# Optimization experiments

Measured on AMD Instinct MI355X. Metric: run time of the kernel, lower is better.

## Reference

```python
import jax, jax.numpy as jnp
import numpy as np

B, N_OBS = 4096, 64
H = 256
SCALE = 0.05  # keep activations stable through SQUARE/MUL layers


def setup_inputs() -> dict:
    key = jax.random.key(0)
    ks = jax.random.split(key, 16)
    rn = lambda k, shp, s=SCALE: s * jax.random.normal(k, shp, dtype=jnp.float32)
    return {
        "x": jax.random.normal(ks[0], (B, N_OBS), dtype=jnp.float32),
        "xdot": jax.random.normal(ks[1], (B, N_OBS), dtype=jnp.float32),
        "w1": rn(ks[2], (H, N_OBS)), "b1": rn(ks[3], (H,)),
        "w2a": rn(ks[4], (H, H)), "b2a": rn(ks[5], (H,)),
        "w2b": rn(ks[6], (H, H)), "b2b": rn(ks[7], (H,)),
        "w3a": rn(ks[8], (H, H)), "b3a": rn(ks[9], (H,)),
        "w3s": rn(ks[10], (H, N_OBS)), "b3s": rn(ks[11], (H,)),
        "wout": rn(ks[12], (1, H)),
        "scalar": jax.random.normal(ks[13], (1,), dtype=jnp.float32),
    }


def reference(x, xdot, w1, b1, w2a, b2a, w2b, b2b, w3a, b3a, w3s, b3s, wout, scalar):
    # mul path: empty mul_activation -> yy = x*0 + scalar  (shape [B, n_obs])
    yy = x * 0 + scalar

    # Layer 1: SQUARE. Initial jac is identity, so
    # matmul(2*diag(z), W1) @ I == 2*z[:,:,None] * W1
    z = x @ w1.T + b1                      # [B, H]
    y = z * z
    jac = (2.0 * z)[:, :, None] * w1[None]  # [B, H, N_OBS]

    # Layer 2: MUL. diag(z1)@W2b + diag(z2)@W2a == z1[:,:,None]*w2b + z2[:,:,None]*w2a
    z1 = y @ w2a.T + b2a
    z2 = y @ w2b.T + b2b
    y = z1 * z2
    grad = z1[:, :, None] * w2b[None] + z2[:, :, None] * w2a[None]  # [B, H, H]
    jac = jnp.einsum('boh,bhi->boi', grad, jac)                      # [B, H, N_OBS]

    # Layer 3: SKIP. jac = diag(z1)@W3s + (diag(z2)@W3a)@jac
    z1 = y @ w3a.T + b3a
    z2 = x @ w3s.T + b3s
    y = z1 * z2
    jac = z1[:, :, None] * w3s[None] + z2[:, :, None] * jnp.einsum('oh,bhi->boi', w3a, jac)

    numerical_b = y @ wout.T                                # [B, 1]
    jac = jnp.einsum('oh,bhi->boi', wout, jac)              # [B, 1, N_OBS]
    numerical_bdot = jnp.sum(jac[:, 0, :] * xdot, axis=1)   # [B]
    return (numerical_b, numerical_bdot, y, yy)
```

## Files before the change

kernel.cpp:

```cpp
#include <hip/hip_runtime.h>

typedef unsigned short ushort_t;
typedef unsigned int uint_t;
typedef __bf16 bf16x8 __attribute__((ext_vector_type(8)));
typedef float f32x4 __attribute__((ext_vector_type(4)));

#define H 256
#define RPB 32
#define NBLK 128

#define NB_OFF 0
#define BDOT_OFF 4096
#define Y_OFF 8192
#define YY_OFF (8192 + 4096 * 256)

__device__ __forceinline__ ushort_t f2bf(float x) {
    union { float f; uint_t u; } c; c.f = x;
    uint_t r = (c.u + 0x7FFFu + ((c.u >> 16) & 1u)) >> 16;
    return (ushort_t)r;
}
__device__ __forceinline__ float bf2f(ushort_t v) {
    union { uint_t u; float f; } c; c.u = ((uint_t)v) << 16;
    return c.f;
}

#define O_W1b  0
#define O_W1T  16384
#define O_W2ab 32768
#define O_W2bb 98304
#define O_W3ab 163840
#define O_W2aT 229376
#define O_W2bT 294912
#define O_W3aT 360448
#define O_W3sb 425984
#define O_W3sT 442368

__global__ __launch_bounds__(256) void prep_weights(
    const float* __restrict__ w1, const float* __restrict__ w2a,
    const float* __restrict__ w2b, const float* __restrict__ w3a,
    const float* __restrict__ w3s, const float* __restrict__ wout,
    ushort_t* __restrict__ ws) {
    __shared__ float tile[32][65];
    int b = blockIdx.x;
    const float* src; int Oo, Ot, C, t; bool scl;
    if (b < 32)       { src = w2a; Oo = O_W2ab; Ot = O_W2aT; C = 256; t = b;       scl = false; }
    else if (b < 64)  { src = w2b; Oo = O_W2bb; Ot = O_W2bT; C = 256; t = b - 32;  scl = false; }
    else if (b < 96)  { src = w3a; Oo = O_W3ab; Ot = O_W3aT; C = 256; t = b - 64;  scl = true;  }
    else if (b < 104) { src = w1;  Oo = O_W1b;  Ot = O_W1T;  C = 64;  t = b - 96;  scl = false; }
    else              { src = w3s; Oo = O_W3sb; Ot = O_W3sT; C = 64;  t = b - 104; scl = true;  }
    int tr, tc;
    if (C == 256) { tr = t >> 2; tc = t & 3; } else { tr = t; tc = 0; }
    int r0 = tr * 32, c0 = tc * 64;
    const int tid = threadIdx.x;

    union pack8 { ushort_t u[8]; uint4 q; };
    {
        int r = tid >> 3, c8 = (tid & 7) << 3;
        const float* s = src + (r0 + r) * C + c0 + c8;
        pack8 p;
#pragma unroll
        for (int j = 0; j < 8; j++) { float v = s[j]; tile[r][c8 + j] = v; p.u[j] = f2bf(v); }
        *(uint4*)(ws + Oo + (r0 + r) * C + c0 + c8) = p.q;
    }
    __syncthreads();
    {
        int cc = tid >> 2, r8 = (tid & 3) << 3;
        pack8 p;
#pragma unroll
        for (int j = 0; j < 8; j++) {
            float v = tile[r8 + j][cc];
            if (scl) v *= wout[r0 + r8 + j];
            p.u[j] = f2bf(v);
        }
        *(uint4*)(ws + Ot + (c0 + cc) * 256 + r0 + r8) = p.q;
    }
}

#define RS 4
#define RA 4
#define U_RING 0
#define U_Y    32768
#define U_Z12  40960
#define U_Z22  49152
#define U_Z23  57344
#define U_U    65536
#define U_XD   73728
#define U_NB   77824
#define SMEM_USHORTS 77888
#define SMEM_BYTES (SMEM_USHORTS * 2)

__device__ __forceinline__ void gload16(const ushort_t* g, ushort_t* l) {
    __builtin_amdgcn_global_load_lds(
        (const __attribute__((address_space(1))) void*)g,
        (__attribute__((address_space(3))) void*)l, 16, 0, 0);
}

template <int N> __device__ __forceinline__ void vwait() {
    if constexpr (N == 3) asm volatile("s_waitcnt vmcnt(3)" ::: "memory");
    else if constexpr (N == 2) asm volatile("s_waitcnt vmcnt(2)" ::: "memory");
    else if constexpr (N == 1) asm volatile("s_waitcnt vmcnt(1)" ::: "memory");
    else asm volatile("s_waitcnt vmcnt(0)" ::: "memory");
}

#define PHASE_BARRIER() do { \
    asm volatile("s_waitcnt lgkmcnt(0)" ::: "memory"); \
    __builtin_amdgcn_sched_barrier(0); \
    __builtin_amdgcn_s_barrier(); \
    __builtin_amdgcn_sched_barrier(0); \
} while (0)

__device__ __forceinline__ int posw(int r, int c) { return r * H + (c ^ ((r & 7) << 3)); }

template <int P, bool SUM>
__device__ __forceinline__ void ring_phase(
    const ushort_t* __restrict__ gm0, const ushort_t* __restrict__ gm1,
    const ushort_t* __restrict__ gn0, const ushort_t* __restrict__ gn1,
    const ushort_t* aM0, const ushort_t* aM1,
    ushort_t* rw, int srcoff, int boff, int kq, int sw,
    f32x4& a00, f32x4& a01, f32x4& a10, f32x4& a11) {
    const int arow0 = ( boff >> 5) * H;
    const int arow1 = arow0 + 16 * H;
#pragma unroll
    for (int k = 0; k < 16; ++k) {
        const int u = P * 16 + k;
        if (P == 2) {
            if (k < 13) vwait<3>();
            else if (k == 13) vwait<2>();
            else if (k == 14) vwait<1>();
            else vwait<0>();
        } else {
            vwait<3>();
        }
        __builtin_amdgcn_sched_barrier(0);
        bf16x8 b = *(const bf16x8*)(rw + (u & 3) * 512 + boff);
        const ushort_t* am = (k & 1) ? aM1 : aM0;
        const int ko = (((k >> 1) << 5) + kq) ^ sw;
        bf16x8 a0 = *(const bf16x8*)(am + arow0 + ko);
        bf16x8 a1 = *(const bf16x8*)(am + arow1 + ko);
        if (u + RA < 48) {
            asm volatile("s_waitcnt lgkmcnt(2)" ::: "memory");
            __builtin_amdgcn_sched_barrier(0);
            const int k4 = k + RA;
            const ushort_t* g = (k4 < 16) ? ((k4 & 1) ? gm1 : gm0)
                                          : ((k4 & 1) ? gn1 : gn0);
            const int cc = (k4 & 15) >> 1;
            gload16(g + srcoff + (cc << 5), rw + ((u + RA) & 3) * 512);
        }
        if ((k & 1) == 0 || SUM) {
            a00 = __builtin_amdgcn_mfma_f32_16x16x32_bf16(a0, b, a00, 0, 0, 0);
            a01 = __builtin_amdgcn_mfma_f32_16x16x32_bf16(a1, b, a01, 0, 0, 0);
        } else {
            a10 = __builtin_amdgcn_mfma_f32_16x16x32_bf16(a0, b, a10, 0, 0, 0);
            a11 = __builtin_amdgcn_mfma_f32_16x16x32_bf16(a1, b, a11, 0, 0, 0);
        }
    }
}

template <int NF, int STRA, int STRB>
__device__ __forceinline__ void gemm_one(const ushort_t* sA, const ushort_t* __restrict__ B0,
                                         int lane, int k0, f32x4& acc0) {
    const int row = lane & 15;
    const int kq = (lane >> 4) << 3;
    const int sw = (row & 7) << 3;
    bf16x8 b0[NF], a[NF];
    const ushort_t* bp0 = B0 + row * STRB + k0 + kq;
    const ushort_t* ap = sA + row * STRA;
#pragma unroll
    for (int i = 0; i < NF; i++) b0[i] = *(const bf16x8*)(bp0 + i * 32);
#pragma unroll
    for (int i = 0; i < NF; i++) a[i] = *(const bf16x8*)(ap + ((k0 + i * 32 + kq) ^ sw));
    __builtin_amdgcn_sched_barrier(0);
#pragma unroll
    for (int i = 0; i < NF; i++)
        acc0 = __builtin_amdgcn_mfma_f32_16x16x32_bf16(a[i], b0[i], acc0, 0, 0, 0);
}

__global__ __launch_bounds__(1024) void net_main(
    const float* __restrict__ x, const float* __restrict__ xd,
    const float* __restrict__ b1, const float* __restrict__ b2a,
    const float* __restrict__ b2b, const float* __restrict__ b3a,
    const float* __restrict__ b3s, const float* __restrict__ wout,
    const float* __restrict__ scalar, const ushort_t* __restrict__ ws,
    float* __restrict__ out) {
    extern __shared__ __align__(16) ushort_t smem[];
    ushort_t* sY   = smem + U_Y;
    ushort_t* sZ12 = smem + U_Z12;
    ushort_t* sZ22 = smem + U_Z22;
    ushort_t* sZ23 = smem + U_Z23;
    ushort_t* sU   = smem + U_U;
    float* sXd = (float*)(smem + U_XD);
    float* sNB = (float*)(smem + U_NB);

    const int tid = threadIdx.x;
    const int wid = tid >> 6;
    const int lane = tid & 63;
    const int row16 = lane & 15;
    const int rq = lane >> 4;
    const int R0 = blockIdx.x * RPB;
    const int n0 = wid * 16;
    const int kq = rq << 3;
    const int sw = (row16 & 7) << 3;

    ushort_t* rw = smem + U_RING + wid * (RS * 512);
    const int nsrc = (wid << 4) + (lane >> 2);
    const int srcoff = nsrc * 256 + (((lane & 3) ^ (nsrc & 3)) << 3);
    const int boff = row16 * 32 + (kq ^ ((row16 & 3) << 3));

    const ushort_t* gW2ab = ws + O_W2ab;
    const ushort_t* gW2bb = ws + O_W2bb;
    const ushort_t* gW3ab = ws + O_W3ab;
    const ushort_t* gW3aT = ws + O_W3aT;
    const ushort_t* gW2bT = ws + O_W2bT;
    const ushort_t* gW2aT = ws + O_W2aT;

    f32x4 zk0, zk1, y3k0, y3k1;

    {
        float sc = scalar[0];
        int xr = tid >> 6, xc = tid & 63;
        float xd0 = xd[(R0 + xr) * 64 + xc];
        float xd1 = xd[(R0 + 16 + xr) * 64 + xc];
        out[YY_OFF + (R0 + xr) * 64 + xc] = sc;
        out[YY_OFF + (R0 + 16 + xr) * 64 + xc] = sc;
        const ushort_t* w1p = ws + O_W1b + (n0 + row16) * 64 + kq;
        const ushort_t* w3p = ws + O_W3sb + (n0 + row16) * 64 + kq;
        bf16x8 pb0 = *(const bf16x8*)(w1p);
        bf16x8 pb1 = *(const bf16x8*)(w1p + 32);
        bf16x8 pb2 = *(const bf16x8*)(w3p);
        bf16x8 pb3 = *(const bf16x8*)(w3p + 32);
        const float* xg0 = x + (R0 + row16) * 64;
        const float* xg1 = x + (R0 + 16 + row16) * 64;
        float4 xa0 = *(const float4*)(xg0 + kq);
        float4 xa1 = *(const float4*)(xg0 + kq + 4);
        float4 xa2 = *(const float4*)(xg0 + 32 + kq);
        float4 xa3 = *(const float4*)(xg0 + 32 + kq + 4);
        float4 xb0 = *(const float4*)(xg1 + kq);
        float4 xb1 = *(const float4*)(xg1 + kq + 4);
        float4 xb2 = *(const float4*)(xg1 + 32 + kq);
        float4 xb3 = *(const float4*)(xg1 + 32 + kq + 4);
        __builtin_amdgcn_sched_barrier(0);
        gload16(gW2ab + srcoff, rw);
        gload16(gW2bb + srcoff, rw + 512);
        gload16(gW2ab + srcoff + 32, rw + 1024);
        gload16(gW2bb + srcoff + 32, rw + 1536);
        __builtin_amdgcn_sched_barrier(0);
        sXd[tid] = xd0;
        sXd[tid + 1024] = xd1;
        if (tid < RPB) sNB[tid] = 0.f;
        union { ushort_t u[8]; bf16x8 v; } A0, A1, B0v, B1v;
#pragma unroll
        for (int j = 0; j < 4; j++) {
            A0.u[j]      = f2bf(((const float*)&xa0)[j]);
            A0.u[4 + j]  = f2bf(((const float*)&xa1)[j]);
            A1.u[j]      = f2bf(((const float*)&xa2)[j]);
            A1.u[4 + j]  = f2bf(((const float*)&xa3)[j]);
            B0v.u[j]     = f2bf(((const float*)&xb0)[j]);
            B0v.u[4 + j] = f2bf(((const float*)&xb1)[j]);
            B1v.u[j]     = f2bf(((const float*)&xb2)[j]);
            B1v.u[4 + j] = f2bf(((const float*)&xb3)[j]);
        }
        f32x4 z0 = {0.f,0.f,0.f,0.f}, z1 = {0.f,0.f,0.f,0.f};
        f32x4 q0 = {0.f,0.f,0.f,0.f}, q1 = {0.f,0.f,0.f,0.f};
        z0 = __builtin_amdgcn_mfma_f32_16x16x32_bf16(A0.v, pb0, z0, 0, 0, 0);
        z0 = __builtin_amdgcn_mfma_f32_16x16x32_bf16(A1.v, pb1, z0, 0, 0, 0);
        z1 = __builtin_amdgcn_mfma_f32_16x16x32_bf16(B0v.v, pb0, z1, 0, 0, 0);
        z1 = __builtin_amdgcn_mfma_f32_16x16x32_bf16(B1v.v, pb1, z1, 0, 0, 0);
        q0 = __builtin_amdgcn_mfma_f32_16x16x32_bf16(A0.v, pb2, q0, 0, 0, 0);
        q0 = __builtin_amdgcn_mfma_f32_16x16x32_bf16(A1.v, pb3, q0, 0, 0, 0);
        q1 = __builtin_amdgcn_mfma_f32_16x16x32_bf16(B0v.v, pb2, q1, 0, 0, 0);
        q1 = __builtin_amdgcn_mfma_f32_16x16x32_bf16(B1v.v, pb3, q1, 0, 0, 0);
        int c = n0 + row16;
        float bz = b1[c], bs = b3s[c];
#pragma unroll
        for (int i = 0; i < 4; i++) {
            int r = rq * 4 + i;
            int p0 = posw(r, c), p1 = posw(r + 16, c);
            float za = z0[i] + bz, zb = z1[i] + bz;
            zk0[i] = za; zk1[i] = zb;
            sY[p0] = f2bf(za * za);
            sY[p1] = f2bf(zb * zb);
            sZ23[p0] = f2bf(q0[i] + bs);
            sZ23[p1] = f2bf(q1[i] + bs);
        }
    }
    PHASE_BARRIER();

    {
        f32x4 a00 = {0.f,0.f,0.f,0.f}, a01 = {0.f,0.f,0.f,0.f};
        f32x4 a10 = {0.f,0.f,0.f,0.f}, a11 = {0.f,0.f,0.f,0.f};
        ring_phase<0, false>(gW2ab, gW2bb, gW3ab, gW3aT, sY, sY,
                             rw, srcoff, boff, kq, sw, a00, a01, a10, a11);
        int c = n0 + row16;
        float ba = b2a[c], bb = b2b[c];
#pragma unroll
        for (int i = 0; i < 4; i++) {
            int r = rq * 4 + i;
            int p0 = posw(r, c), p1 = posw(r + 16, c);
            float z12a = a00[i] + ba, z22a = a10[i] + bb;
            float z12b = a01[i] + ba, z22b = a11[i] + bb;
            sZ12[p0] = f2bf(z12a); sZ22[p0] = f2bf(z22a); sU[p0] = f2bf(z12a * z22a);
            sZ12[p1] = f2bf(z12b); sZ22[p1] = f2bf(z22b); sU[p1] = f2bf(z12b * z22b);
        }
    }
    PHASE_BARRIER();

    {
        f32x4 zz0 = {0.f,0.f,0.f,0.f}, zz1 = {0.f,0.f,0.f,0.f};
        f32x4 tt0 = {0.f,0.f,0.f,0.f}, tt1 = {0.f,0.f,0.f,0.f};
        ring_phase<1, false>(gW3ab, gW3aT, gW2bT, gW2aT, sU, sZ23,
                             rw, srcoff, boff, kq, sw, zz0, zz1, tt0, tt1);
        int c = n0 + row16;
        float ba = b3a[c], wo = wout[c];
#pragma unroll
        for (int i = 0; i < 4; i++) {
            int r = rq * 4 + i;
            int p0 = posw(r, c), p1 = posw(r + 16, c);
            float z13a = zz0[i] + ba, z23a = bf2f(sZ23[p0]);
            float z13b = zz1[i] + ba, z23b = bf2f(sZ23[p1]);
            float y3a = z13a * z23a, y3b = z13b * z23b;
            y3k0[i] = y3a; y3k1[i] = y3b;
            sY[p0] = f2bf(z13a);
            sY[p1] = f2bf(z13b);
            sZ12[p0] = f2bf(tt0[i] * bf2f(sZ12[p0]));
            sZ22[p0] = f2bf(tt0[i] * bf2f(sZ22[p0]));
            sZ12[p1] = f2bf(tt1[i] * bf2f(sZ12[p1]));
            sZ22[p1] = f2bf(tt1[i] * bf2f(sZ22[p1]));
            float v0 = wo * y3a, v1 = wo * y3b;
            v0 += __shfl_xor(v0, 1); v0 += __shfl_xor(v0, 2);
            v0 += __shfl_xor(v0, 4); v0 += __shfl_xor(v0, 8);
            v1 += __shfl_xor(v1, 1); v1 += __shfl_xor(v1, 2);
            v1 += __shfl_xor(v1, 4); v1 += __shfl_xor(v1, 8);
            if (row16 == 0) { atomicAdd(&sNB[r], v0); atomicAdd(&sNB[r + 16], v1); }
        }
    }
    PHASE_BARRIER();

    {
        f32x4 pp0 = {0.f,0.f,0.f,0.f}, pp1 = {0.f,0.f,0.f,0.f};
        f32x4 d0 = {0.f,0.f,0.f,0.f}, d1 = {0.f,0.f,0.f,0.f};
        ring_phase<2, true>(gW2bT, gW2aT, gW2bT, gW2aT, sZ12, sZ22,
                            rw, srcoff, boff, kq, sw, pp0, pp1, d0, d1);
        int c = n0 + row16;
#pragma unroll
        for (int i = 0; i < 4; i++) {
            int r = rq * 4 + i;
            sU[posw(r, c)] = f2bf(2.f * pp0[i] * zk0[i]);
            sU[posw(r + 16, c)] = f2bf(2.f * pp1[i] * zk1[i]);
        }
    }
    PHASE_BARRIER();

    {
        int c = n0 + row16;
#pragma unroll
        for (int i = 0; i < 4; i++) {
            out[Y_OFF + (R0 + rq * 4 + i) * H + c] = y3k0[i];
            out[Y_OFF + (R0 + 16 + rq * 4 + i) * H + c] = y3k1[i];
        }
        int mat = wid >> 3, kh = (wid >> 2) & 1, nt = wid & 3;
        const ushort_t* Abase = mat ? sU : sY;
        const ushort_t* B = ws + (mat ? O_W1T : O_W3sT) + nt * 16 * H;
        float* dst = (float*)(mat ? sZ22 : sZ12) + kh * 2048;
        int cc = nt * 16 + row16;
#pragma unroll
        for (int rg = 0; rg < 2; rg++) {
            f32x4 acc = {0.f,0.f,0.f,0.f};
            gemm_one<4, H, H>(Abase + rg * 16 * H, B, lane, kh * 128, acc);
#pragma unroll
            for (int i = 0; i < 4; i++)
                dst[(rg * 16 + rq * 4 + i) * 64 + cc] = acc[i];
        }
    }
    PHASE_BARRIER();

    {
        float* F0 = (float*)sZ12;
        float* F1 = F0 + 2048;
        float* F2 = (float*)sZ22;
        float* F3 = F2 + 2048;
        int r = tid >> 5, j = tid & 31;
        int e = r * 64 + j, e2 = e + 32;
        float s = (F0[e] + F1[e] + F2[e] + F3[e]) * sXd[e] +
                  (F0[e2] + F1[e2] + F2[e2] + F3[e2]) * sXd[e2];
        s += __shfl_xor(s, 1);
        s += __shfl_xor(s, 2);
        s += __shfl_xor(s, 4);
        s += __shfl_xor(s, 8);
        s += __shfl_xor(s, 16);
        if (j == 0) out[BDOT_OFF + R0 + r] = s;
        if (tid < RPB) out[NB_OFF + R0 + tid] = sNB[tid];
    }
}

extern "C" void kernel_launch(void* const* d_in, const int* in_sizes, int n_in,
                              void* d_out, int out_size, void* d_ws, size_t ws_size,
                              hipStream_t stream) {
    (void)in_sizes; (void)n_in; (void)out_size; (void)ws_size;
    const float* x = (const float*)d_in[0];
    const float* xd = (const float*)d_in[1];
    const float* w1 = (const float*)d_in[2];
    const float* b1 = (const float*)d_in[3];
    const float* w2a = (const float*)d_in[4];
    const float* b2a = (const float*)d_in[5];
    const float* w2b = (const float*)d_in[6];
    const float* b2b = (const float*)d_in[7];
    const float* w3a = (const float*)d_in[8];
    const float* b3a = (const float*)d_in[9];
    const float* w3s = (const float*)d_in[10];
    const float* b3s = (const float*)d_in[11];
    const float* wout = (const float*)d_in[12];
    const float* scalar = (const float*)d_in[13];
    ushort_t* ws = (ushort_t*)d_ws;
    float* out = (float*)d_out;

    static bool attr_set = false;
    if (!attr_set) {
        hipFuncSetAttribute((const void*)net_main,
                            hipFuncAttributeMaxDynamicSharedMemorySize, SMEM_BYTES);
        attr_set = true;
    }

    prep_weights<<<112, 256, 0, stream>>>(w1, w2a, w2b, w3a, w3s, wout, ws);
    net_main<<<NBLK, 1024, SMEM_BYTES, stream>>>(x, xd, b1, b2a, b2b, b3a, b3s, wout, scalar, ws, out);
}
```

Baseline: 35.33 us.

## Split each row tile across paired blocks exchanging partials via global flags

The grid doubles from 128 to 256 blocks. Each 32-row tile is now handled by a pair of blocks, one for the even (z1) matrices and one for the odd (z2) matrices. The two blocks exchange intermediates (y1, z22, t, z13, partial products, partial Jacobian) through a global workspace and synchronise with acquire/release flags that prep_weights clears. The aim is to halve per-block GEMM work and use more compute units, at the cost of global-memory round trips, spin-waiting, and a deadlock risk if the paired blocks are not co-resident.

```diff
diff --git a/kernel.cpp b/kernel.cpp
--- a/kernel.cpp
+++ b/kernel.cpp
@@ -7,7 +7,8 @@
 
 #define H 256
 #define RPB 32
-#define NBLK 128
+#define PAIRS 128
+#define NBLK 256
 
 #define NB_OFF 0
 #define BDOT_OFF 4096
@@ -34,14 +35,36 @@
 #define O_W3aT 360448
 #define O_W3sb 425984
 #define O_W3sT 442368
+#define X_EX   458752
+#define PXU    61440
+#define EX_Y1  0
+#define EX_Z23 8192
+#define EX_Z22 16384
+#define EX_T   24576
+#define EX_Z13 32768
+#define EX_PO  40960
+#define EX_FJ  57344
+#define X_FLAG (X_EX + PAIRS * PXU)
+#define FE1 0
+#define FE2 1
+#define FO2 2
+#define FO3 3
+#define FO4 4
+#define FO5 5
 
 __global__ __launch_bounds__(256) void prep_weights(
     const float* __restrict__ w1, const float* __restrict__ w2a,
     const float* __restrict__ w2b, const float* __restrict__ w3a,
     const float* __restrict__ w3s, const float* __restrict__ wout,
     ushort_t* __restrict__ ws) {
+    int b = blockIdx.x;
+    const int tid = threadIdx.x;
+    if (b == 112) {
+        int* fl = (int*)(ws + X_FLAG);
+        for (int i = tid; i < PAIRS * 8; i += 256) fl[i] = 0;
+        return;
+    }
     __shared__ float tile[32][65];
-    int b = blockIdx.x;
     const float* src; int Oo, Ot, C, t; bool scl;
     if (b < 32)       { src = w2a; Oo = O_W2ab; Ot = O_W2aT; C = 256; t = b;       scl = false; }
     else if (b < 64)  { src = w2b; Oo = O_W2bb; Ot = O_W2bT; C = 256; t = b - 32;  scl = false; }
@@ -51,7 +74,6 @@
     int tr, tc;
     if (C == 256) { tr = t >> 2; tc = t & 3; } else { tr = t; tc = 0; }
     int r0 = tr * 32, c0 = tc * 64;
-    const int tid = threadIdx.x;
 
     union pack8 { ushort_t u[8]; uint4 q; };
     {
@@ -76,17 +98,13 @@
     }
 }
 
-#define RS 4
-#define RA 4
 #define U_RING 0
-#define U_Y    32768
-#define U_Z12  40960
-#define U_Z22  49152
-#define U_Z23  57344
-#define U_U    65536
-#define U_XD   73728
-#define U_NB   77824
-#define SMEM_USHORTS 77888
+#define U_B0   32768
+#define U_B1   40960
+#define U_B2   49152
+#define U_XD   57344
+#define U_NB   61440
+#define SMEM_USHORTS 61504
 #define SMEM_BYTES (SMEM_USHORTS * 2)
 
 __device__ __forceinline__ void gload16(const ushort_t* g, ushort_t* l) {
@@ -109,50 +127,54 @@
     __builtin_amdgcn_sched_barrier(0); \
 } while (0)
 
+__device__ __forceinline__ void post_flag(int* f) {
+    __syncthreads();
+    if (threadIdx.x == 0)
+        __hip_atomic_store(f, 1, __ATOMIC_RELEASE, __HIP_MEMORY_SCOPE_AGENT);
+}
+__device__ __forceinline__ void wait_flag(int* f) {
+    if (threadIdx.x == 0) {
+        while (__hip_atomic_load(f, __ATOMIC_ACQUIRE, __HIP_MEMORY_SCOPE_AGENT) == 0)
+            __builtin_amdgcn_s_sleep(2);
+    }
+    __syncthreads();
+}
+
 __device__ __forceinline__ int posw(int r, int c) { return r * H + (c ^ ((r & 7) << 3)); }
 
-template <int P, bool SUM>
-__device__ __forceinline__ void ring_phase(
-    const ushort_t* __restrict__ gm0, const ushort_t* __restrict__ gm1,
-    const ushort_t* __restrict__ gn0, const ushort_t* __restrict__ gn1,
-    const ushort_t* aM0, const ushort_t* aM1,
-    ushort_t* rw, int srcoff, int boff, int kq, int sw,
-    f32x4& a00, f32x4& a01, f32x4& a10, f32x4& a11) {
-    const int arow0 = ( boff >> 5) * H;
+template <int PH>
+__device__ __forceinline__ void ring8(
+    const ushort_t* __restrict__ mA, const ushort_t* __restrict__ mB,
+    const ushort_t* __restrict__ mC,
+    const ushort_t* aM, ushort_t* rw, int srcoff, int boff, int row16,
+    int kq, int sw, f32x4& acc0, f32x4& acc1) {
+    const int arow0 = row16 * H;
     const int arow1 = arow0 + 16 * H;
 #pragma unroll
-    for (int k = 0; k < 16; ++k) {
-        const int u = P * 16 + k;
-        if (P == 2) {
-            if (k < 13) vwait<3>();
-            else if (k == 13) vwait<2>();
-            else if (k == 14) vwait<1>();
+    for (int k = 0; k < 8; ++k) {
+        const int u = PH * 8 + k;
+        if (PH == 2) {
+            if (k < 5) vwait<3>();
+            else if (k == 5) vwait<2>();
+            else if (k == 6) vwait<1>();
             else vwait<0>();
         } else {
             vwait<3>();
         }
         __builtin_amdgcn_sched_barrier(0);
         bf16x8 b = *(const bf16x8*)(rw + (u & 3) * 512 + boff);
-        const ushort_t* am = (k & 1) ? aM1 : aM0;
-        const int ko = (((k >> 1) << 5) + kq) ^ sw;
-        bf16x8 a0 = *(const bf16x8*)(am + arow0 + ko);
-        bf16x8 a1 = *(const bf16x8*)(am + arow1 + ko);
-        if (u + RA < 48) {
+        const int ko = ((k << 5) + kq) ^ sw;
+        bf16x8 a0 = *(const bf16x8*)(aM + arow0 + ko);
+        bf16x8 a1 = *(const bf16x8*)(aM + arow1 + ko);
+        if (u + 4 < 24) {
             asm volatile("s_waitcnt lgkmcnt(2)" ::: "memory");
             __builtin_amdgcn_sched_barrier(0);
-            const int k4 = k + RA;
-            const ushort_t* g = (k4 < 16) ? ((k4 & 1) ? gm1 : gm0)
-                                          : ((k4 & 1) ? gn1 : gn0);
-            const int cc = (k4 & 15) >> 1;
-            gload16(g + srcoff + (cc << 5), rw + ((u + RA) & 3) * 512);
-        }
-        if ((k & 1) == 0 || SUM) {
-            a00 = __builtin_amdgcn_mfma_f32_16x16x32_bf16(a0, b, a00, 0, 0, 0);
-            a01 = __builtin_amdgcn_mfma_f32_16x16x32_bf16(a1, b, a01, 0, 0, 0);
-        } else {
-            a10 = __builtin_amdgcn_mfma_f32_16x16x32_bf16(a0, b, a10, 0, 0, 0);
-            a11 = __builtin_amdgcn_mfma_f32_16x16x32_bf16(a1, b, a11, 0, 0, 0);
-        }
+            const int u4 = u + 4;
+            const ushort_t* g = (u4 < 8) ? mA : (u4 < 16) ? mB : mC;
+            gload16(g + srcoff + ((u4 & 7) << 5), rw + (u4 & 3) * 512);
+        }
+        acc0 = __builtin_amdgcn_mfma_f32_16x16x32_bf16(a0, b, acc0, 0, 0, 0);
+        acc1 = __builtin_amdgcn_mfma_f32_16x16x32_bf16(a1, b, acc1, 0, 0, 0);
     }
 }
 
@@ -180,215 +202,338 @@
     const float* __restrict__ b1, const float* __restrict__ b2a,
     const float* __restrict__ b2b, const float* __restrict__ b3a,
     const float* __restrict__ b3s, const float* __restrict__ wout,
-    const float* __restrict__ scalar, const ushort_t* __restrict__ ws,
+    const float* __restrict__ scalar, ushort_t* __restrict__ ws,
     float* __restrict__ out) {
     extern __shared__ __align__(16) ushort_t smem[];
-    ushort_t* sY   = smem + U_Y;
-    ushort_t* sZ12 = smem + U_Z12;
-    ushort_t* sZ22 = smem + U_Z22;
-    ushort_t* sZ23 = smem + U_Z23;
-    ushort_t* sU   = smem + U_U;
+    ushort_t* sB0 = smem + U_B0;
+    ushort_t* sB1 = smem + U_B1;
+    ushort_t* sB2 = smem + U_B2;
     float* sXd = (float*)(smem + U_XD);
     float* sNB = (float*)(smem + U_NB);
+    float* sFJ = (float*)smem;
 
     const int tid = threadIdx.x;
     const int wid = tid >> 6;
     const int lane = tid & 63;
     const int row16 = lane & 15;
     const int rq = lane >> 4;
-    const int R0 = blockIdx.x * RPB;
+    const bool isE = blockIdx.x < PAIRS;
+    const int pid = blockIdx.x & (PAIRS - 1);
+    const int R0 = pid * RPB;
     const int n0 = wid * 16;
     const int kq = rq << 3;
     const int sw = (row16 & 7) << 3;
 
-    ushort_t* rw = smem + U_RING + wid * (RS * 512);
+    ushort_t* rw = smem + U_RING + wid * 2048;
     const int nsrc = (wid << 4) + (lane >> 2);
     const int srcoff = nsrc * 256 + (((lane & 3) ^ (nsrc & 3)) << 3);
     const int boff = row16 * 32 + (kq ^ ((row16 & 3) << 3));
 
-    const ushort_t* gW2ab = ws + O_W2ab;
-    const ushort_t* gW2bb = ws + O_W2bb;
-    const ushort_t* gW3ab = ws + O_W3ab;
-    const ushort_t* gW3aT = ws + O_W3aT;
-    const ushort_t* gW2bT = ws + O_W2bT;
-    const ushort_t* gW2aT = ws + O_W2aT;
-
-    f32x4 zk0, zk1, y3k0, y3k1;
-
-    {
-        float sc = scalar[0];
-        int xr = tid >> 6, xc = tid & 63;
-        float xd0 = xd[(R0 + xr) * 64 + xc];
-        float xd1 = xd[(R0 + 16 + xr) * 64 + xc];
-        out[YY_OFF + (R0 + xr) * 64 + xc] = sc;
-        out[YY_OFF + (R0 + 16 + xr) * 64 + xc] = sc;
-        const ushort_t* w1p = ws + O_W1b + (n0 + row16) * 64 + kq;
-        const ushort_t* w3p = ws + O_W3sb + (n0 + row16) * 64 + kq;
-        bf16x8 pb0 = *(const bf16x8*)(w1p);
-        bf16x8 pb1 = *(const bf16x8*)(w1p + 32);
-        bf16x8 pb2 = *(const bf16x8*)(w3p);
-        bf16x8 pb3 = *(const bf16x8*)(w3p + 32);
-        const float* xg0 = x + (R0 + row16) * 64;
-        const float* xg1 = x + (R0 + 16 + row16) * 64;
-        float4 xa0 = *(const float4*)(xg0 + kq);
-        float4 xa1 = *(const float4*)(xg0 + kq + 4);
-        float4 xa2 = *(const float4*)(xg0 + 32 + kq);
-        float4 xa3 = *(const float4*)(xg0 + 32 + kq + 4);
-        float4 xb0 = *(const float4*)(xg1 + kq);
-        float4 xb1 = *(const float4*)(xg1 + kq + 4);
-        float4 xb2 = *(const float4*)(xg1 + 32 + kq);
-        float4 xb3 = *(const float4*)(xg1 + 32 + kq + 4);
-        __builtin_amdgcn_sched_barrier(0);
-        gload16(gW2ab + srcoff, rw);
-        gload16(gW2bb + srcoff, rw + 512);
-        gload16(gW2ab + srcoff + 32, rw + 1024);
-        gload16(gW2bb + srcoff + 32, rw + 1536);
-        __builtin_amdgcn_sched_barrier(0);
-        sXd[tid] = xd0;
-        sXd[tid + 1024] = xd1;
-        if (tid < RPB) sNB[tid] = 0.f;
-        union { ushort_t u[8]; bf16x8 v; } A0, A1, B0v, B1v;
-#pragma unroll
-        for (int j = 0; j < 4; j++) {
-            A0.u[j]      = f2bf(((const float*)&xa0)[j]);
-            A0.u[4 + j]  = f2bf(((const float*)&xa1)[j]);
-            A1.u[j]      = f2bf(((const float*)&xa2)[j]);
-            A1.u[4 + j]  = f2bf(((const float*)&xa3)[j]);
-            B0v.u[j]     = f2bf(((const float*)&xb0)[j]);
-            B0v.u[4 + j] = f2bf(((const float*)&xb1)[j]);
-            B1v.u[j]     = f2bf(((const float*)&xb2)[j]);
-            B1v.u[4 + j] = f2bf(((const float*)&xb3)[j]);
-        }
-        f32x4 z0 = {0.f,0.f,0.f,0.f}, z1 = {0.f,0.f,0.f,0.f};
-        f32x4 q0 = {0.f,0.f,0.f,0.f}, q1 = {0.f,0.f,0.f,0.f};
-        z0 = __builtin_amdgcn_mfma_f32_16x16x32_bf16(A0.v, pb0, z0, 0, 0, 0);
-        z0 = __builtin_amdgcn_mfma_f32_16x16x32_bf16(A1.v, pb1, z0, 0, 0, 0);
-        z1 = __builtin_amdgcn_mfma_f32_16x16x32_bf16(B0v.v, pb0, z1, 0, 0, 0);
-        z1 = __builtin_amdgcn_mfma_f32_16x16x32_bf16(B1v.v, pb1, z1, 0, 0, 0);
-        q0 = __builtin_amdgcn_mfma_f32_16x16x32_bf16(A0.v, pb2, q0, 0, 0, 0);
-        q0 = __builtin_amdgcn_mfma_f32_16x16x32_bf16(A1.v, pb3, q0, 0, 0, 0);
-        q1 = __builtin_amdgcn_mfma_f32_16x16x32_bf16(B0v.v, pb2, q1, 0, 0, 0);
-        q1 = __builtin_amdgcn_mfma_f32_16x16x32_bf16(B1v.v, pb3, q1, 0, 0, 0);
-        int c = n0 + row16;
-        float bz = b1[c], bs = b3s[c];
-#pragma unroll
-        for (int i = 0; i < 4; i++) {
-            int r = rq * 4 + i;
-            int p0 = posw(r, c), p1 = posw(r + 16, c);
-            float za = z0[i] + bz, zb = z1[i] + bz;
-            zk0[i] = za; zk1[i] = zb;
-            sY[p0] = f2bf(za * za);
-            sY[p1] = f2bf(zb * zb);
-            sZ23[p0] = f2bf(q0[i] + bs);
-            sZ23[p1] = f2bf(q1[i] + bs);
-        }
-    }
-    PHASE_BARRIER();
-
-    {
-        f32x4 a00 = {0.f,0.f,0.f,0.f}, a01 = {0.f,0.f,0.f,0.f};
-        f32x4 a10 = {0.f,0.f,0.f,0.f}, a11 = {0.f,0.f,0.f,0.f};
-        ring_phase<0, false>(gW2ab, gW2bb, gW3ab, gW3aT, sY, sY,
-                             rw, srcoff, boff, kq, sw, a00, a01, a10, a11);
-        int c = n0 + row16;
-        float ba = b2a[c], bb = b2b[c];
-#pragma unroll
-        for (int i = 0; i < 4; i++) {
-            int r = rq * 4 + i;
-            int p0 = posw(r, c), p1 = posw(r + 16, c);
-            float z12a = a00[i] + ba, z22a = a10[i] + bb;
-            float z12b = a01[i] + ba, z22b = a11[i] + bb;
-            sZ12[p0] = f2bf(z12a); sZ22[p0] = f2bf(z22a); sU[p0] = f2bf(z12a * z22a);
-            sZ12[p1] = f2bf(z12b); sZ22[p1] = f2bf(z22b); sU[p1] = f2bf(z12b * z22b);
-        }
-    }
-    PHASE_BARRIER();
-
-    {
-        f32x4 zz0 = {0.f,0.f,0.f,0.f}, zz1 = {0.f,0.f,0.f,0.f};
-        f32x4 tt0 = {0.f,0.f,0.f,0.f}, tt1 = {0.f,0.f,0.f,0.f};
-        ring_phase<1, false>(gW3ab, gW3aT, gW2bT, gW2aT, sU, sZ23,
-                             rw, srcoff, boff, kq, sw, zz0, zz1, tt0, tt1);
-        int c = n0 + row16;
-        float ba = b3a[c], wo = wout[c];
-#pragma unroll
-        for (int i = 0; i < 4; i++) {
-            int r = rq * 4 + i;
-            int p0 = posw(r, c), p1 = posw(r + 16, c);
-            float z13a = zz0[i] + ba, z23a = bf2f(sZ23[p0]);
-            float z13b = zz1[i] + ba, z23b = bf2f(sZ23[p1]);
-            float y3a = z13a * z23a, y3b = z13b * z23b;
-            y3k0[i] = y3a; y3k1[i] = y3b;
-            sY[p0] = f2bf(z13a);
-            sY[p1] = f2bf(z13b);
-            sZ12[p0] = f2bf(tt0[i] * bf2f(sZ12[p0]));
-            sZ22[p0] = f2bf(tt0[i] * bf2f(sZ22[p0]));
-            sZ12[p1] = f2bf(tt1[i] * bf2f(sZ12[p1]));
-            sZ22[p1] = f2bf(tt1[i] * bf2f(sZ22[p1]));
-            float v0 = wo * y3a, v1 = wo * y3b;
-            v0 += __shfl_xor(v0, 1); v0 += __shfl_xor(v0, 2);
-            v0 += __shfl_xor(v0, 4); v0 += __shfl_xor(v0, 8);
-            v1 += __shfl_xor(v1, 1); v1 += __shfl_xor(v1, 2);
-            v1 += __shfl_xor(v1, 4); v1 += __shfl_xor(v1, 8);
-            if (row16 == 0) { atomicAdd(&sNB[r], v0); atomicAdd(&sNB[r + 16], v1); }
-        }
-    }
-    PHASE_BARRIER();
-
-    {
-        f32x4 pp0 = {0.f,0.f,0.f,0.f}, pp1 = {0.f,0.f,0.f,0.f};
-        f32x4 d0 = {0.f,0.f,0.f,0.f}, d1 = {0.f,0.f,0.f,0.f};
-        ring_phase<2, true>(gW2bT, gW2aT, gW2bT, gW2aT, sZ12, sZ22,
-                            rw, srcoff, boff, kq, sw, pp0, pp1, d0, d1);
-        int c = n0 + row16;
-#pragma unroll
-        for (int i = 0; i < 4; i++) {
-            int r = rq * 4 + i;
-            sU[posw(r, c)] = f2bf(2.f * pp0[i] * zk0[i]);
-            sU[posw(r + 16, c)] = f2bf(2.f * pp1[i] * zk1[i]);
-        }
-    }
-    PHASE_BARRIER();
-
-    {
-        int c = n0 + row16;
-#pragma unroll
-        for (int i = 0; i < 4; i++) {
-            out[Y_OFF + (R0 + rq * 4 + i) * H + c] = y3k0[i];
-            out[Y_OFF + (R0 + 16 + rq * 4 + i) * H + c] = y3k1[i];
-        }
-        int mat = wid >> 3, kh = (wid >> 2) & 1, nt = wid & 3;
-        const ushort_t* Abase = mat ? sU : sY;
-        const ushort_t* B = ws + (mat ? O_W1T : O_W3sT) + nt * 16 * H;
-        float* dst = (float*)(mat ? sZ22 : sZ12) + kh * 2048;
-        int cc = nt * 16 + row16;
-#pragma unroll
-        for (int rg = 0; rg < 2; rg++) {
-            f32x4 acc = {0.f,0.f,0.f,0.f};
-            gemm_one<4, H, H>(Abase + rg * 16 * H, B, lane, kh * 128, acc);
-#pragma unroll
-            for (int i = 0; i < 4; i++)
-                dst[(rg * 16 + rq * 4 + i) * 64 + cc] = acc[i];
-        }
-    }
-    PHASE_BARRIER();
-
-    {
-        float* F0 = (float*)sZ12;
-        float* F1 = F0 + 2048;
-        float* F2 = (float*)sZ22;
-        float* F3 = F2 + 2048;
-        int r = tid >> 5, j = tid & 31;
-        int e = r * 64 + j, e2 = e + 32;
-        float s = (F0[e] + F1[e] + F2[e] + F3[e]) * sXd[e] +
-                  (F0[e2] + F1[e2] + F2[e2] + F3[e2]) * sXd[e2];
-        s += __shfl_xor(s, 1);
-        s += __shfl_xor(s, 2);
-        s += __shfl_xor(s, 4);
-        s += __shfl_xor(s, 8);
-        s += __shfl_xor(s, 16);
-        if (j == 0) out[BDOT_OFF + R0 + r] = s;
-        if (tid < RPB) out[NB_OFF + R0 + tid] = sNB[tid];
+    ushort_t* ex = ws + X_EX + pid * PXU;
+    int* fl = (int*)(ws + X_FLAG) + pid * 8;
+
+    const int c = n0 + row16;
+
+    if (isE) {
+        const ushort_t* m0 = ws + O_W2ab;
+        const ushort_t* m1 = ws + O_W3ab;
+        const ushort_t* m2 = ws + O_W2bT;
+        f32x4 zk0, zk1;
+        {
+            const ushort_t* w1p = ws + O_W1b + c * 64 + kq;
+            bf16x8 pb0 = *(const bf16x8*)(w1p);
+            bf16x8 pb1 = *(const bf16x8*)(w1p + 32);
+            const float* xg0 = x + (R0 + row16) * 64;
+            const float* xg1 = x + (R0 + 16 + row16) * 64;
+            float4 xa0 = *(const float4*)(xg0 + kq);
+            float4 xa1 = *(const float4*)(xg0 + kq + 4);
+            float4 xa2 = *(const float4*)(xg0 + 32 + kq);
+            float4 xa3 = *(const float4*)(xg0 + 32 + kq + 4);
+            float4 xb0 = *(const float4*)(xg1 + kq);
+            float4 xb1 = *(const float4*)(xg1 + kq + 4);
+            float4 xb2 = *(const float4*)(xg1 + 32 + kq);
+            float4 xb3 = *(const float4*)(xg1 + 32 + kq + 4);
+            gload16(m0 + srcoff, rw);
+            gload16(m0 + srcoff + 32, rw + 512);
+            gload16(m0 + srcoff + 64, rw + 1024);
+            gload16(m0 + srcoff + 96, rw + 1536);
+            float sc = scalar[0];
+            {
+                int xr = tid >> 6, xc = tid & 63;
+                sXd[tid] = xd[(R0 + xr) * 64 + xc];
+                sXd[tid + 1024] = xd[(R0 + 16 + xr) * 64 + xc];
+                out[YY_OFF + (R0 + xr) * 64 + xc] = sc;
+                out[YY_OFF + (R0 + 16 + xr) * 64 + xc] = sc;
+                if (tid < RPB) sNB[tid] = 0.f;
+            }
+            union { ushort_t u[8]; bf16x8 v; } A0, A1, B0, B1;
+#pragma unroll
+            for (int j = 0; j < 4; j++) {
+                A0.u[j] = f2bf(((const float*)&xa0)[j]);
+                A0.u[4 + j] = f2bf(((const float*)&xa1)[j]);
+                A1.u[j] = f2bf(((const float*)&xa2)[j]);
+                A1.u[4 + j] = f2bf(((const float*)&xa3)[j]);
+                B0.u[j] = f2bf(((const float*)&xb0)[j]);
+                B0.u[4 + j] = f2bf(((const float*)&xb1)[j]);
+                B1.u[j] = f2bf(((const float*)&xb2)[j]);
+                B1.u[4 + j] = f2bf(((const float*)&xb3)[j]);
+            }
+            f32x4 z0 = {0.f,0.f,0.f,0.f}, z1 = {0.f,0.f,0.f,0.f};
+            z0 = __builtin_amdgcn_mfma_f32_16x16x32_bf16(A0.v, pb0, z0, 0, 0, 0);
+            z0 = __builtin_amdgcn_mfma_f32_16x16x32_bf16(A1.v, pb1, z0, 0, 0, 0);
+            z1 = __builtin_amdgcn_mfma_f32_16x16x32_bf16(B0.v, pb0, z1, 0, 0, 0);
+            z1 = __builtin_amdgcn_mfma_f32_16x16x32_bf16(B1.v, pb1, z1, 0, 0, 0);
+            float bz = b1[c];
+#pragma unroll
+            for (int i = 0; i < 4; i++) {
+                int r = rq * 4 + i;
+                float za = z0[i] + bz, zb = z1[i] + bz;
+                zk0[i] = za; zk1[i] = zb;
+                ushort_t ya = f2bf(za * za), yb = f2bf(zb * zb);
+                sB0[posw(r, c)] = ya; sB0[posw(r + 16, c)] = yb;
+                ex[EX_Y1 + r * H + c] = ya;
+                ex[EX_Y1 + (r + 16) * H + c] = yb;
+            }
+        }
+        post_flag(fl + FE1);
+
+        {
+            f32x4 a0 = {0.f,0.f,0.f,0.f}, a1 = {0.f,0.f,0.f,0.f};
+            ring8<0>(m0, m1, m2, sB0, rw, srcoff, boff, row16, kq, sw, a0, a1);
+            float ba = b2a[c];
+#pragma unroll
+            for (int i = 0; i < 4; i++) {
+                int r = rq * 4 + i;
+                sB1[posw(r, c)] = f2bf(a0[i] + ba);
+                sB1[posw(r + 16, c)] = f2bf(a1[i] + ba);
+            }
+        }
+        PHASE_BARRIER();
+        wait_flag(fl + FO2);
+        for (int e = tid; e < RPB * H; e += 1024) {
+            int r = e >> 8, cc2 = e & 255;
+            float z22 = bf2f(ex[EX_Z22 + e]);
+            int p = posw(r, cc2);
+            sB0[p] = f2bf(bf2f(sB1[p]) * z22);
+        }
+        PHASE_BARRIER();
+
+        f32x4 y3k0, y3k1;
+        {
+            f32x4 z0 = {0.f,0.f,0.f,0.f}, z1 = {0.f,0.f,0.f,0.f};
+            ring8<1>(m0, m1, m2, sB0, rw, srcoff, boff, row16, kq, sw, z0, z1);
+            float ba = b3a[c], wo = wout[c];
+#pragma unroll
+            for (int i = 0; i < 4; i++) {
+                int r = rq * 4 + i;
+                float z13a = z0[i] + ba, z13b = z1[i] + ba;
+                float z23a = bf2f(ex[EX_Z23 + r * H + c]);
+                float z23b = bf2f(ex[EX_Z23 + (r + 16) * H + c]);
+                float y3a = z13a * z23a, y3b = z13b * z23b;
+                y3k0[i] = y3a; y3k1[i] = y3b;
+                out[Y_OFF + (R0 + r) * H + c] = y3a;
+                out[Y_OFF + (R0 + 16 + r) * H + c] = y3b;
+                ex[EX_Z13 + r * H + c] = f2bf(z13a);
+                ex[EX_Z13 + (r + 16) * H + c] = f2bf(z13b);
+                float v0 = wo * y3a, v1 = wo * y3b;
+                v0 += __shfl_xor(v0, 1); v0 += __shfl_xor(v0, 2);
+                v0 += __shfl_xor(v0, 4); v0 += __shfl_xor(v0, 8);
+                v1 += __shfl_xor(v1, 1); v1 += __shfl_xor(v1, 2);
+                v1 += __shfl_xor(v1, 4); v1 += __shfl_xor(v1, 8);
+                if (row16 == 0) { atomicAdd(&sNB[r], v0); atomicAdd(&sNB[r + 16], v1); }
+            }
+        }
+        post_flag(fl + FE2);
+        wait_flag(fl + FO3);
+        {
+#pragma unroll
+            for (int i = 0; i < 4; i++) {
+                int r = rq * 4 + i;
+                int p0 = posw(r, c), p1 = posw(r + 16, c);
+                float t0 = bf2f(ex[EX_T + r * H + c]);
+                float t1 = bf2f(ex[EX_T + (r + 16) * H + c]);
+                sB1[p0] = f2bf(t0 * bf2f(sB1[p0]));
+                sB1[p1] = f2bf(t1 * bf2f(sB1[p1]));
+            }
+        }
+        PHASE_BARRIER();
+
+        {
+            f32x4 p0 = {0.f,0.f,0.f,0.f}, p1 = {0.f,0.f,0.f,0.f};
+            ring8<2>(m0, m1, m2, sB1, rw, srcoff, boff, row16, kq, sw, p0, p1);
+            wait_flag(fl + FO4);
+            const float* poF = (const float*)(ex + EX_PO);
+#pragma unroll
+            for (int i = 0; i < 4; i++) {
+                int r = rq * 4 + i;
+                float pa = p0[i] + poF[r * H + c];
+                float pb = p1[i] + poF[(r + 16) * H + c];
+                sB1[posw(r, c)] = f2bf(2.f * pa * zk0[i]);
+                sB1[posw(r + 16, c)] = f2bf(2.f * pb * zk1[i]);
+            }
+        }
+        PHASE_BARRIER();
+
+        {
+            int nt = wid & 3, kh = wid >> 2;
+            const ushort_t* B = ws + O_W1T + nt * 16 * H;
+            int cc2 = nt * 16 + row16;
+#pragma unroll
+            for (int rg = 0; rg < 2; rg++) {
+                f32x4 acc = {0.f,0.f,0.f,0.f};
+                gemm_one<2, H, H>(sB1 + rg * 16 * H, B, lane, kh * 64, acc);
+#pragma unroll
+                for (int i = 0; i < 4; i++)
+                    sFJ[kh * 2048 + (rg * 16 + rq * 4 + i) * 64 + cc2] = acc[i];
+            }
+        }
+        PHASE_BARRIER();
+        wait_flag(fl + FO5);
+        {
+            const float* fjO = (const float*)(ex + EX_FJ);
+            int r = tid >> 5, j = tid & 31;
+            int e = r * 64 + j, e2 = e + 32;
+            float s = (sFJ[e] + sFJ[2048 + e] + sFJ[4096 + e] + sFJ[6144 + e] + fjO[e]) * sXd[e] +
+                      (sFJ[e2] + sFJ[2048 + e2] + sFJ[4096 + e2] + sFJ[6144 + e2] + fjO[e2]) * sXd[e2];
+            s += __shfl_xor(s, 1);
+            s += __shfl_xor(s, 2);
+            s += __shfl_xor(s, 4);
+            s += __shfl_xor(s, 8);
+            s += __shfl_xor(s, 16);
+            if (j == 0) out[BDOT_OFF + R0 + r] = s;
+            if (tid < RPB) out[NB_OFF + R0 + tid] = sNB[tid];
+        }
+    } else {
+        const ushort_t* m0 = ws + O_W2bb;
+        const ushort_t* m1 = ws + O_W3aT;
+        const ushort_t* m2 = ws + O_W2aT;
+        {
+            const ushort_t* w3p = ws + O_W3sb + c * 64 + kq;
+            bf16x8 pb0 = *(const bf16x8*)(w3p);
+            bf16x8 pb1 = *(const bf16x8*)(w3p + 32);
+            const float* xg0 = x + (R0 + row16) * 64;
+            const float* xg1 = x + (R0 + 16 + row16) * 64;
+            float4 xa0 = *(const float4*)(xg0 + kq);
+            float4 xa1 = *(const float4*)(xg0 + kq + 4);
+            float4 xa2 = *(const float4*)(xg0 + 32 + kq);
+            float4 xa3 = *(const float4*)(xg0 + 32 + kq + 4);
+            float4 xb0 = *(const float4*)(xg1 + kq);
+            float4 xb1 = *(const float4*)(xg1 + kq + 4);
+            float4 xb2 = *(const float4*)(xg1 + 32 + kq);
+            float4 xb3 = *(const float4*)(xg1 + 32 + kq + 4);
+            gload16(m0 + srcoff, rw);
+            gload16(m0 + srcoff + 32, rw + 512);
+            gload16(m0 + srcoff + 64, rw + 1024);
+            gload16(m0 + srcoff + 96, rw + 1536);
+            union { ushort_t u[8]; bf16x8 v; } A0, A1, B0, B1;
+#pragma unroll
+            for (int j = 0; j < 4; j++) {
+                A0.u[j] = f2bf(((const float*)&xa0)[j]);
+                A0.u[4 + j] = f2bf(((const float*)&xa1)[j]);
+                A1.u[j] = f2bf(((const float*)&xa2)[j]);
+                A1.u[4 + j] = f2bf(((const float*)&xa3)[j]);
+                B0.u[j] = f2bf(((const float*)&xb0)[j]);
+                B0.u[4 + j] = f2bf(((const float*)&xb1)[j]);
+                B1.u[j] = f2bf(((const float*)&xb2)[j]);
+                B1.u[4 + j] = f2bf(((const float*)&xb3)[j]);
+            }
+            f32x4 q0 = {0.f,0.f,0.f,0.f}, q1 = {0.f,0.f,0.f,0.f};
+            q0 = __builtin_amdgcn_mfma_f32_16x16x32_bf16(A0.v, pb0, q0, 0, 0, 0);
+            q0 = __builtin_amdgcn_mfma_f32_16x16x32_bf16(A1.v, pb1, q0, 0, 0, 0);
+            q1 = __builtin_amdgcn_mfma_f32_16x16x32_bf16(B0.v, pb0, q1, 0, 0, 0);
+            q1 = __builtin_amdgcn_mfma_f32_16x16x32_bf16(B1.v, pb1, q1, 0, 0, 0);
+            float bs = b3s[c];
+#pragma unroll
+            for (int i = 0; i < 4; i++) {
+                int r = rq * 4 + i;
+                ushort_t va = f2bf(q0[i] + bs), vb = f2bf(q1[i] + bs);
+                sB1[posw(r, c)] = va; sB1[posw(r + 16, c)] = vb;
+                ex[EX_Z23 + r * H + c] = va;
+                ex[EX_Z23 + (r + 16) * H + c] = vb;
+            }
+        }
+        wait_flag(fl + FE1);
+        for (int e = tid; e < RPB * H; e += 1024) {
+            int r = e >> 8, cc2 = e & 255;
+            sB0[posw(r, cc2)] = ex[EX_Y1 + e];
+        }
+        PHASE_BARRIER();
+
+        {
+            f32x4 a0 = {0.f,0.f,0.f,0.f}, a1 = {0.f,0.f,0.f,0.f};
+            ring8<0>(m0, m1, m2, sB0, rw, srcoff, boff, row16, kq, sw, a0, a1);
+            float bb = b2b[c];
+#pragma unroll
+            for (int i = 0; i < 4; i++) {
+                int r = rq * 4 + i;
+                ushort_t va = f2bf(a0[i] + bb), vb = f2bf(a1[i] + bb);
+                sB2[posw(r, c)] = va; sB2[posw(r + 16, c)] = vb;
+                ex[EX_Z22 + r * H + c] = va;
+                ex[EX_Z22 + (r + 16) * H + c] = vb;
+            }
+        }
+        post_flag(fl + FO2);
+        PHASE_BARRIER();
+
+        {
+            f32x4 t0 = {0.f,0.f,0.f,0.f}, t1 = {0.f,0.f,0.f,0.f};
+            ring8<1>(m0, m1, m2, sB1, rw, srcoff, boff, row16, kq, sw, t0, t1);
+#pragma unroll
+            for (int i = 0; i < 4; i++) {
+                int r = rq * 4 + i;
+                ex[EX_T + r * H + c] = f2bf(t0[i]);
+                ex[EX_T + (r + 16) * H + c] = f2bf(t1[i]);
+            }
+            post_flag(fl + FO3);
+#pragma unroll
+            for (int i = 0; i < 4; i++) {
+                int r = rq * 4 + i;
+                int p0 = posw(r, c), p1 = posw(r + 16, c);
+                sB2[p0] = f2bf(t0[i] * bf2f(sB2[p0]));
+                sB2[p1] = f2bf(t1[i] * bf2f(sB2[p1]));
+            }
+        }
+        PHASE_BARRIER();
+
+        {
+            f32x4 p0 = {0.f,0.f,0.f,0.f}, p1 = {0.f,0.f,0.f,0.f};
+            ring8<2>(m0, m1, m2, sB2, rw, srcoff, boff, row16, kq, sw, p0, p1);
+            float* poF = (float*)(ex + EX_PO);
+#pragma unroll
+            for (int i = 0; i < 4; i++) {
+                int r = rq * 4 + i;
+                poF[r * H + c] = p0[i];
+                poF[(r + 16) * H + c] = p1[i];
+            }
+        }
+        post_flag(fl + FO4);
+        wait_flag(fl + FE2);
+        for (int e = tid; e < RPB * H; e += 1024) {
+            int r = e >> 8, cc2 = e & 255;
+            sB0[posw(r, cc2)] = ex[EX_Z13 + e];
+        }
+        PHASE_BARRIER();
+
+        {
+            int nt = wid & 3, kh = wid >> 2;
+            const ushort_t* B = ws + O_W3sT + nt * 16 * H;
+            int cc2 = nt * 16 + row16;
+#pragma unroll
+            for (int rg = 0; rg < 2; rg++) {
+                f32x4 acc = {0.f,0.f,0.f,0.f};
+                gemm_one<2, H, H>(sB0 + rg * 16 * H, B, lane, kh * 64, acc);
+#pragma unroll
+                for (int i = 0; i < 4; i++)
+                    sFJ[kh * 2048 + (rg * 16 + rq * 4 + i) * 64 + cc2] = acc[i];
+            }
+        }
+        PHASE_BARRIER();
+        {
+            float* fjO = (float*)(ex + EX_FJ);
+            for (int e = tid; e < 2048; e += 1024)
+                fjO[e] = sFJ[e] + sFJ[2048 + e] + sFJ[4096 + e] + sFJ[6144 + e];
+        }
+        post_flag(fl + FO5);
     }
 }
 
@@ -420,6 +565,6 @@
         attr_set = true;
     }
 
-    prep_weights<<<112, 256, 0, stream>>>(w1, w2a, w2b, w3a, w3s, wout, ws);
+    prep_weights<<<113, 256, 0, stream>>>(w1, w2a, w2b, w3a, w3s, wout, ws);
     net_main<<<NBLK, 1024, SMEM_BYTES, stream>>>(x, xd, b1, b2a, b2b, b3a, b3s, wout, scalar, ws, out);
 }
```

Result: slower. 76.50 us (+116.6%).
